# Optimization experiments

Measured on AMD Instinct MI355X. Metric: run time of the kernel, lower is better.

## Reference

```python
import jax, jax.numpy as jnp
import numpy as np

DIM = 4096
N_HEADS_Q = 32
N_HEADS_KV = 8
N_REP = N_HEADS_Q // N_HEADS_KV
HEAD_DIM = DIM // N_HEADS_Q


def setup_inputs() -> dict:
    key = jax.random.key(0)
    k0, k1, k2, k3, k4 = jax.random.split(key, 5)
    B, S = 2, 2048
    scale = 1.0 / np.sqrt(DIM)
    return {
        "x": jax.random.normal(k0, (B, S, DIM), dtype=jnp.float32),
        "wq": jax.random.normal(k1, (DIM, N_HEADS_Q * HEAD_DIM), dtype=jnp.float32) * scale,
        "wk": jax.random.normal(k2, (DIM, N_HEADS_KV * HEAD_DIM), dtype=jnp.float32) * scale,
        "wv": jax.random.normal(k3, (DIM, N_HEADS_KV * HEAD_DIM), dtype=jnp.float32) * scale,
        "wo": jax.random.normal(k4, (DIM, DIM), dtype=jnp.float32) * scale,
        "start_pos": 0,
    }


def reference(x, wq, wk, wv, wo, start_pos):
    # use_cache=False path: fresh causal self-attention with GQA.
    B, S, _ = x.shape
    q = (x @ wq).reshape(B, S, N_HEADS_Q, HEAD_DIM)
    k = (x @ wk).reshape(B, S, N_HEADS_KV, HEAD_DIM)
    v = (x @ wv).reshape(B, S, N_HEADS_KV, HEAD_DIM)
    # repeat_kv: each kv head repeated N_REP times contiguously along head axis
    k = jnp.repeat(k, N_REP, axis=2)  # [B, S, Hq, D]
    v = jnp.repeat(v, N_REP, axis=2)
    att = jnp.einsum("bqhd,bkhd->bhqk", q, k) / np.sqrt(HEAD_DIM).astype(np.float32)
    causal = jnp.tril(jnp.ones((S, S), dtype=bool))  # [S, S]
    att = jnp.where(causal[None, None, :, :], att, -jnp.inf)
    scores = jax.nn.softmax(att, axis=-1)
    out = jnp.einsum("bhqk,bkhd->bqhd", scores, v).reshape(B, S, DIM)
    return out @ wo
```

## Files before the change

kernel.cpp:

```cpp
#include <hip/hip_runtime.h>
#include <cstdint>


typedef __bf16 bf16;
typedef __bf16 bf16x8 __attribute__((ext_vector_type(8)));
typedef float f32x4 __attribute__((ext_vector_type(4)));

#define DEV_INLINE __device__ __forceinline__

DEV_INLINE void load_lds16(const bf16* g, bf16* l) {
  __builtin_amdgcn_global_load_lds(
      (const __attribute__((address_space(1))) void*)g,
      (__attribute__((address_space(3))) void*)l, 16, 0, 0);
}

__global__ __launch_bounds__(256) void cast_f32_bf16(const float* __restrict__ in,
                                                     bf16* __restrict__ out, int n) {
  int i = (blockIdx.x * 256 + threadIdx.x) * 8;
  if (i >= n) return;
  float4 a = *(const float4*)(in + i);
  float4 b = *(const float4*)(in + i + 4);
  bf16x8 o;
  o[0] = (bf16)a.x; o[1] = (bf16)a.y; o[2] = (bf16)a.z; o[3] = (bf16)a.w;
  o[4] = (bf16)b.x; o[5] = (bf16)b.y; o[6] = (bf16)b.z; o[7] = (bf16)b.w;
  *(bf16x8*)(out + i) = o;
}

__global__ __launch_bounds__(256) void transpose_cast_all(
    const float* __restrict__ wq, const float* __restrict__ wk,
    const float* __restrict__ wv, const float* __restrict__ wo,
    bf16* __restrict__ wt, bf16* __restrict__ wot, float qscale) {
  __shared__ float t[32][33];
  int bx = blockIdx.x, k0 = blockIdx.y * 32;
  const float* src;
  bf16* dst;
  int N, ncol0, nrow0;
  float scale = 1.0f;
  if (bx < 128) {
    src = wq; dst = wt; N = 4096; ncol0 = bx * 32; nrow0 = ncol0; scale = qscale;
  } else if (bx < 160) {
    src = wk; dst = wt; N = 1024; ncol0 = (bx - 128) * 32; nrow0 = 4096 + ncol0;
  } else if (bx < 192) {
    src = wv; dst = wt; N = 1024; ncol0 = (bx - 160) * 32; nrow0 = 5120 + ncol0;
  } else {
    src = wo; dst = wot; N = 4096; ncol0 = (bx - 192) * 32; nrow0 = ncol0;
  }
  int tx = threadIdx.x, ty = threadIdx.y;
#pragma unroll
  for (int i = 0; i < 32; i += 8)
    t[ty + i][tx] = src[(size_t)(k0 + ty + i) * N + ncol0 + tx];
  __syncthreads();
#pragma unroll
  for (int i = 0; i < 32; i += 8)
    dst[(size_t)(nrow0 + ty + i) * 4096 + k0 + tx] = (bf16)(t[tx][ty + i] * scale);
}

__global__ __launch_bounds__(256) void transpose_v(const bf16* __restrict__ qkv,
                                                   bf16* __restrict__ vt) {
  __shared__ bf16 t[32][33];
  int s0 = blockIdx.x * 32, d0 = blockIdx.y * 32, bh = blockIdx.z;
  int b = bh >> 3, h = bh & 7;
  int tx = threadIdx.x, ty = threadIdx.y;
#pragma unroll
  for (int i = 0; i < 32; i += 8)
    t[ty + i][tx] =
        qkv[(size_t)(b * 2048 + s0 + ty + i) * 6144 + 5120 + h * 128 + d0 + tx];
  __syncthreads();
#pragma unroll
  for (int i = 0; i < 32; i += 8)
    vt[((size_t)bh * 128 + d0 + ty + i) * 2048 + s0 + tx] = t[tx][ty + i];
}

template <typename OT>
__global__ __launch_bounds__(512, 2) void gemm_bt8(const bf16* __restrict__ A,
                                                   const bf16* __restrict__ Bt,
                                                   OT* __restrict__ C,
                                                   int M, int N, int K) {
  __shared__ __align__(16) bf16 lds[2][4][128 * 64];
  const int t = threadIdx.x, w = t >> 6, l = t & 63;
  const int lr = l & 15, lh = l >> 4;
  const int rm = w >> 2, cn = w & 3;
  const int mBase = blockIdx.y * 256, nBase = blockIdx.x * 256;
  const int NT = K >> 6;

  size_t gA0[2], gB0[2];
#pragma unroll
  for (int it = 0; it < 2; it++) {
    int c = it * 512 + t;
    int idx = c >> 3;
    int kc = (c & 7) ^ (idx & 7);
    gA0[it] = (size_t)(mBase + (idx >> 6) * 128 + (idx & 63)) * K + kc * 8;
    gB0[it] = (size_t)(nBase + (idx >> 5) * 64 + (idx & 31)) * K + kc * 8;
  }
  const size_t strideA1 = (size_t)64 * K;
  const size_t strideB1 = (size_t)32 * K;
  const int ldst0 = (w * 64) * 8, ldst1 = (512 + w * 64) * 8;

#define STAGE_Q(tile, q, base, off0, off1)                                  \
  do {                                                                      \
    int th_ = (tile);                                                       \
    if (th_ < NT) {                                                         \
      bf16* qb_ = &lds[th_ & 1][q][0];                                      \
      size_t ka_ = (size_t)th_ * 64;                                        \
      load_lds16((base) + (off0) + ka_, qb_ + ldst0);                       \
      load_lds16((base) + (off1) + ka_, qb_ + ldst1);                       \
    }                                                                       \
  } while (0)
#define STAGE_A0(tile) STAGE_Q(tile, 0, A, gA0[0], gA0[1])
#define STAGE_B0(tile) STAGE_Q(tile, 1, Bt, gB0[0], gB0[1])
#define STAGE_B1(tile) STAGE_Q(tile, 2, Bt, gB0[0] + strideB1, gB0[1] + strideB1)
#define STAGE_A1(tile) STAGE_Q(tile, 3, A, gA0[0] + strideA1, gA0[1] + strideA1)

  STAGE_A0(0); STAGE_B0(0); STAGE_B1(0); STAGE_A1(0);
  STAGE_A0(1); STAGE_B0(1); STAGE_B1(1);

  f32x4 acc[8][4] = {};
  bf16x8 aF[4][2], bF[4][2];
  const int rowA = (rm * 64 + lr) * 64;
  const int colB = (cn * 32 + lr) * 64;
  const int xo0 = ((lh ^ (lr & 7)) << 3);
  const int xo1 = (((4 + lh) ^ (lr & 7)) << 3);

  for (int T = 0; T < NT; T++) {
    if (T < NT - 1) asm volatile("s_waitcnt vmcnt(6)" ::: "memory");
    else            asm volatile("s_waitcnt vmcnt(0)" ::: "memory");
    __builtin_amdgcn_s_barrier();
    const bf16* q0 = &lds[T & 1][0][0];
    const bf16* q1 = &lds[T & 1][1][0];
    const bf16* q2 = &lds[T & 1][2][0];
    const bf16* q3 = &lds[T & 1][3][0];

#pragma unroll
    for (int mi = 0; mi < 4; mi++) {
      aF[mi][0] = *(const bf16x8*)(q0 + rowA + mi * 1024 + xo0);
      aF[mi][1] = *(const bf16x8*)(q0 + rowA + mi * 1024 + xo1);
    }
#pragma unroll
    for (int ni = 0; ni < 2; ni++) {
      bF[ni][0] = *(const bf16x8*)(q1 + colB + ni * 1024 + xo0);
      bF[ni][1] = *(const bf16x8*)(q1 + colB + ni * 1024 + xo1);
    }
    STAGE_A1(T + 1);
    asm volatile("s_waitcnt lgkmcnt(8)" ::: "memory");
    __builtin_amdgcn_s_barrier();
    asm volatile("s_waitcnt lgkmcnt(0)" ::: "memory");
    __builtin_amdgcn_sched_barrier(0);
    __builtin_amdgcn_s_setprio(1);
#pragma unroll
    for (int mi = 0; mi < 4; mi++)
#pragma unroll
      for (int ni = 0; ni < 2; ni++) {
        acc[mi][ni] = __builtin_amdgcn_mfma_f32_16x16x32_bf16(aF[mi][0], bF[ni][0], acc[mi][ni], 0, 0, 0);
        acc[mi][ni] = __builtin_amdgcn_mfma_f32_16x16x32_bf16(aF[mi][1], bF[ni][1], acc[mi][ni], 0, 0, 0);
      }
    __builtin_amdgcn_s_setprio(0);
    __builtin_amdgcn_s_barrier();

#pragma unroll
    for (int ni = 0; ni < 2; ni++) {
      bF[2 + ni][0] = *(const bf16x8*)(q2 + colB + ni * 1024 + xo0);
      bF[2 + ni][1] = *(const bf16x8*)(q2 + colB + ni * 1024 + xo1);
    }
    STAGE_A0(T + 2);
    __builtin_amdgcn_s_barrier();
    asm volatile("s_waitcnt lgkmcnt(0)" ::: "memory");
    __builtin_amdgcn_sched_barrier(0);
    __builtin_amdgcn_s_setprio(1);
#pragma unroll
    for (int mi = 0; mi < 4; mi++)
#pragma unroll
      for (int ni = 2; ni < 4; ni++) {
        acc[mi][ni] = __builtin_amdgcn_mfma_f32_16x16x32_bf16(aF[mi][0], bF[ni][0], acc[mi][ni], 0, 0, 0);
        acc[mi][ni] = __builtin_amdgcn_mfma_f32_16x16x32_bf16(aF[mi][1], bF[ni][1], acc[mi][ni], 0, 0, 0);
      }
    __builtin_amdgcn_s_setprio(0);
    __builtin_amdgcn_s_barrier();

#pragma unroll
    for (int mi = 0; mi < 4; mi++) {
      aF[mi][0] = *(const bf16x8*)(q3 + rowA + mi * 1024 + xo0);
      aF[mi][1] = *(const bf16x8*)(q3 + rowA + mi * 1024 + xo1);
    }
    STAGE_B0(T + 2);
    __builtin_amdgcn_s_barrier();
    asm volatile("s_waitcnt lgkmcnt(0)" ::: "memory");
    __builtin_amdgcn_sched_barrier(0);
    __builtin_amdgcn_s_setprio(1);
#pragma unroll
    for (int mi = 0; mi < 4; mi++)
#pragma unroll
      for (int ni = 0; ni < 2; ni++) {
        acc[4 + mi][ni] = __builtin_amdgcn_mfma_f32_16x16x32_bf16(aF[mi][0], bF[ni][0], acc[4 + mi][ni], 0, 0, 0);
        acc[4 + mi][ni] = __builtin_amdgcn_mfma_f32_16x16x32_bf16(aF[mi][1], bF[ni][1], acc[4 + mi][ni], 0, 0, 0);
      }
    __builtin_amdgcn_s_setprio(0);
    __builtin_amdgcn_s_barrier();

    STAGE_B1(T + 2);
    __builtin_amdgcn_s_barrier();
    __builtin_amdgcn_s_setprio(1);
#pragma unroll
    for (int mi = 0; mi < 4; mi++)
#pragma unroll
      for (int ni = 2; ni < 4; ni++) {
        acc[4 + mi][ni] = __builtin_amdgcn_mfma_f32_16x16x32_bf16(aF[mi][0], bF[ni][0], acc[4 + mi][ni], 0, 0, 0);
        acc[4 + mi][ni] = __builtin_amdgcn_mfma_f32_16x16x32_bf16(aF[mi][1], bF[ni][1], acc[4 + mi][ni], 0, 0, 0);
      }
    __builtin_amdgcn_s_setprio(0);
    __builtin_amdgcn_s_barrier();
  }
#undef STAGE_Q
#undef STAGE_A0
#undef STAGE_B0
#undef STAGE_B1
#undef STAGE_A1

#pragma unroll
  for (int mi = 0; mi < 8; mi++)
#pragma unroll
    for (int ni = 0; ni < 4; ni++) {
      int row = mBase + rm * 128 + mi * 16 + lh * 4;
      int col = nBase + cn * 64 + ni * 16 + lr;
#pragma unroll
      for (int r = 0; r < 4; r++)
        C[(size_t)(row + r) * N + col] = (OT)acc[mi][ni][r];
    }
}

__global__ __launch_bounds__(256, 2) void flash_attn(const bf16* __restrict__ qkv,
                                                     const bf16* __restrict__ vt,
                                                     bf16* __restrict__ ao) {
  __shared__ __align__(16) bf16 Ks[2][64 * 128];
  __shared__ __align__(16) bf16 Vts[2][128 * 64];
  __shared__ __align__(16) bf16 Ps[4][32 * 64];
  const int t = threadIdx.x, w = t >> 6, l = t & 63;
  const int lr = l & 15, lh = l >> 4;
  const int h = blockIdx.y, b = blockIdx.z;
  const int hkv = h >> 2;

#define STAGE_KV(kt_, buf_)                                                   \
  do {                                                                        \
    const int kb_ = (kt_) * 64;                                               \
    _Pragma("unroll")                                                         \
    for (int p = 0; p < 4; p++) {                                             \
      int c = p * 256 + t;                                                    \
      int ldsoff = (p * 256 + w * 64) * 8;                                    \
      int krow = c >> 4, kj = (c & 15) ^ (krow & 15);                         \
      load_lds16(qkv + (size_t)(b * 2048 + kb_ + krow) * 6144 + 4096 +        \
                     hkv * 128 + kj * 8,                                      \
                 &Ks[buf_][ldsoff]);                                          \
      int vrow = c >> 3, vj = (c & 7) ^ (vrow & 7);                           \
      load_lds16(vt + ((size_t)(b * 8 + hkv) * 128 + vrow) * 2048 + kb_ +     \
                     vj * 8,                                                  \
                 &Vts[buf_][ldsoff]);                                         \
    }                                                                         \
  } while (0)

  for (int phase = 0; phase < 2; phase++) {
    const int qt = phase == 0 ? blockIdx.x : 15 - blockIdx.x;
    const int qrow0 = qt * 128 + w * 32;
    const int nkt = 2 * qt + 2;

    STAGE_KV(0, 0);

    bf16x8 qf[2][4];
#pragma unroll
    for (int rt = 0; rt < 2; rt++)
#pragma unroll
      for (int ds = 0; ds < 4; ds++)
        qf[rt][ds] = *(const bf16x8*)&qkv[(size_t)(b * 2048 + qrow0 + rt * 16 + lr) * 6144 +
                                          h * 128 + ds * 32 + lh * 8];

    f32x4 oacc[2][8] = {};
    float mrow[2][4], lsum[2][4];
#pragma unroll
    for (int rt = 0; rt < 2; rt++)
#pragma unroll
      for (int r = 0; r < 4; r++) { mrow[rt][r] = -3.0e38f; lsum[rt][r] = 0.f; }

    asm volatile("s_waitcnt vmcnt(0)" ::: "memory");
    __builtin_amdgcn_s_barrier();

    for (int kt = 0; kt < nkt; kt++) {
      const int cur = kt & 1;
      const int kbase = kt * 64;
      if (kt + 1 < nkt) STAGE_KV(kt + 1, cur ^ 1);

      f32x4 s[2][4];
      __builtin_amdgcn_s_setprio(1);
#pragma unroll
      for (int ct = 0; ct < 4; ct++) {
        bf16x8 kf[4];
#pragma unroll
        for (int ds = 0; ds < 4; ds++)
          kf[ds] = *(const bf16x8*)&Ks[cur][((ct * 16 + lr) * 16 + ((ds * 4 + lh) ^ lr)) * 8];
#pragma unroll
        for (int rt = 0; rt < 2; rt++) {
          f32x4 acc = {0.f, 0.f, 0.f, 0.f};
#pragma unroll
          for (int ds = 0; ds < 4; ds++)
            acc = __builtin_amdgcn_mfma_f32_16x16x32_bf16(qf[rt][ds], kf[ds], acc, 0, 0, 0);
          s[rt][ct] = acc;
        }
      }
      __builtin_amdgcn_s_setprio(0);

      if (kt >= 2 * qt) {
#pragma unroll
        for (int rt = 0; rt < 2; rt++)
#pragma unroll
          for (int ct = 0; ct < 4; ct++)
#pragma unroll
            for (int r = 0; r < 4; r++) {
              int qi = qrow0 + rt * 16 + lh * 4 + r;
              int ki = kbase + ct * 16 + lr;
              if (ki > qi) s[rt][ct][r] = -3.0e38f;
            }
      }

      float alpha[2][4];
#pragma unroll
      for (int rt = 0; rt < 2; rt++)
#pragma unroll
        for (int r = 0; r < 4; r++) {
          float mx = fmaxf(fmaxf(s[rt][0][r], s[rt][1][r]),
                           fmaxf(s[rt][2][r], s[rt][3][r]));
          mx = fmaxf(mx, __shfl_xor(mx, 1));
          mx = fmaxf(mx, __shfl_xor(mx, 2));
          mx = fmaxf(mx, __shfl_xor(mx, 4));
          mx = fmaxf(mx, __shfl_xor(mx, 8));
          float mnew = fmaxf(mrow[rt][r], mx);
          float al = exp2f(mrow[rt][r] - mnew);
          mrow[rt][r] = mnew;
          alpha[rt][r] = al;
          float rs = 0.f;
#pragma unroll
          for (int ct = 0; ct < 4; ct++) {
            float p = exp2f(s[rt][ct][r] - mnew);
            s[rt][ct][r] = p;
            rs += p;
          }
          rs += __shfl_xor(rs, 1);
          rs += __shfl_xor(rs, 2);
          rs += __shfl_xor(rs, 4);
          rs += __shfl_xor(rs, 8);
          lsum[rt][r] = lsum[rt][r] * al + rs;
        }

#pragma unroll
      for (int rt = 0; rt < 2; rt++)
#pragma unroll
        for (int dt = 0; dt < 8; dt++)
#pragma unroll
          for (int r = 0; r < 4; r++) oacc[rt][dt][r] *= alpha[rt][r];

#pragma unroll
      for (int rt = 0; rt < 2; rt++)
#pragma unroll
        for (int ct = 0; ct < 4; ct++)
#pragma unroll
          for (int r = 0; r < 4; r++) {
            int row = rt * 16 + lh * 4 + r;
            int col = ct * 16 + lr;
            Ps[w][row * 64 + ((((col >> 3) ^ (row & 7)) << 3) | (col & 7))] =
                (bf16)s[rt][ct][r];
          }
      bf16x8 pf[2][2];
#pragma unroll
      for (int rt = 0; rt < 2; rt++)
#pragma unroll
        for (int ks = 0; ks < 2; ks++)
          pf[rt][ks] = *(const bf16x8*)&Ps[w][(rt * 16 + lr) * 64 +
                                              (((ks * 4 + lh) ^ (lr & 7)) << 3)];

      __builtin_amdgcn_s_setprio(1);
#pragma unroll
      for (int dt = 0; dt < 8; dt++)
#pragma unroll
        for (int ks = 0; ks < 2; ks++) {
          bf16x8 vf = *(const bf16x8*)&Vts[cur][((dt * 16 + lr) * 8 +
                                                 ((ks * 4 + lh) ^ (lr & 7))) * 8];
#pragma unroll
          for (int rt = 0; rt < 2; rt++)
            oacc[rt][dt] =
                __builtin_amdgcn_mfma_f32_16x16x32_bf16(pf[rt][ks], vf, oacc[rt][dt], 0, 0, 0);
        }
      __builtin_amdgcn_s_setprio(0);

      asm volatile("s_waitcnt vmcnt(0)" ::: "memory");
      __builtin_amdgcn_s_barrier();
    }

#pragma unroll
    for (int rt = 0; rt < 2; rt++)
#pragma unroll
      for (int dt = 0; dt < 8; dt++)
#pragma unroll
        for (int r = 0; r < 4; r++) {
          float o = oacc[rt][dt][r] / lsum[rt][r];
          int row = b * 2048 + qrow0 + rt * 16 + lh * 4 + r;
          int col = h * 128 + dt * 16 + lr;
          ao[(size_t)row * 4096 + col] = (bf16)o;
        }
  }
#undef STAGE_KV
}

extern "C" void kernel_launch(void* const* d_in, const int* in_sizes, int n_in,
                              void* d_out, int out_size, void* d_ws, size_t ws_size,
                              hipStream_t stream) {
  const float* x = (const float*)d_in[0];
  const float* wq = (const float*)d_in[1];
  const float* wk = (const float*)d_in[2];
  const float* wv = (const float*)d_in[3];
  const float* wo = (const float*)d_in[4];
  float* out = (float*)d_out;

  char* ws = (char*)d_ws;
  bf16* xb = (bf16*)(ws + 0);
  bf16* wt = (bf16*)(ws + 33554432);
  bf16* wot = (bf16*)(ws + 83886080);
  bf16* qkv = (bf16*)(ws + 117440512);
  bf16* vt = (bf16*)(ws + 167772160);
  bf16* ao = (bf16*)(ws + 176160768);
  if (ws_size < 209715200u) return;

  const float qscale = 0.08838834764831845f * 1.4426950408889634f;

  cast_f32_bf16<<<8192, 256, 0, stream>>>(x, xb, 16777216);
  transpose_cast_all<<<dim3(320, 128), dim3(32, 8), 0, stream>>>(
      wq, wk, wv, wo, wt, wot, qscale);

  gemm_bt8<bf16><<<dim3(24, 16), 512, 0, stream>>>(xb, wt, qkv, 4096, 6144, 4096);
  transpose_v<<<dim3(64, 4, 16), dim3(32, 8), 0, stream>>>(qkv, vt);
  flash_attn<<<dim3(8, 32, 2), 256, 0, stream>>>(qkv, vt, ao);
  gemm_bt8<float><<<dim3(16, 16), 512, 0, stream>>>(ao, wot, out, 4096, 4096, 4096);
}
```

Baseline: 790.3 us.

## Rewrite flash attention with transposed 32x32x16 MFMA and register-resident P

Restructures the attention inner loop to compute S^T = K·Q^T with 32x32x16 bf16 MFMAs, so each lane owns one query row. Row max and sum become mostly in-register reductions plus a single cross-half shuffle. P is repacked into MFMA operand layout with lane shuffles, which removes the per-warp LDS round trip. Output stores become 4-wide vectors. The cost is larger accumulators (f32x16 per tile), which adds register pressure at two blocks per CU.

Result: faster. 686.6 us (-13.1%).

```diff
diff --git a/kernel.cpp b/kernel.cpp
--- a/kernel.cpp
+++ b/kernel.cpp
@@ -3,8 +3,10 @@
 
 
 typedef __bf16 bf16;
+typedef __bf16 bf16x4 __attribute__((ext_vector_type(4)));
 typedef __bf16 bf16x8 __attribute__((ext_vector_type(8)));
 typedef float f32x4 __attribute__((ext_vector_type(4)));
+typedef float f32x16 __attribute__((ext_vector_type(16)));
 
 #define DEV_INLINE __device__ __forceinline__
 
@@ -12,6 +14,12 @@
   __builtin_amdgcn_global_load_lds(
       (const __attribute__((address_space(1))) void*)g,
       (__attribute__((address_space(3))) void*)l, 16, 0, 0);
+}
+
+DEV_INLINE unsigned pk2(float a, float b) {
+  union { bf16 v[2]; unsigned u; } t;
+  t.v[0] = (bf16)a; t.v[1] = (bf16)b;
+  return t.u;
 }
 
 __global__ __launch_bounds__(256) void cast_f32_bf16(const float* __restrict__ in,
@@ -232,9 +240,8 @@
                                                      bf16* __restrict__ ao) {
   __shared__ __align__(16) bf16 Ks[2][64 * 128];
   __shared__ __align__(16) bf16 Vts[2][128 * 64];
-  __shared__ __align__(16) bf16 Ps[4][32 * 64];
   const int t = threadIdx.x, w = t >> 6, l = t & 63;
-  const int lr = l & 15, lh = l >> 4;
+  const int l31 = l & 31, hi = l >> 5;
   const int h = blockIdx.y, b = blockIdx.z;
   const int hkv = h >> 2;
 
@@ -260,23 +267,18 @@
     const int qt = phase == 0 ? blockIdx.x : 15 - blockIdx.x;
     const int qrow0 = qt * 128 + w * 32;
     const int nkt = 2 * qt + 2;
+    const int q = qrow0 + l31;
 
     STAGE_KV(0, 0);
 
-    bf16x8 qf[2][4];
-#pragma unroll
-    for (int rt = 0; rt < 2; rt++)
-#pragma unroll
-      for (int ds = 0; ds < 4; ds++)
-        qf[rt][ds] = *(const bf16x8*)&qkv[(size_t)(b * 2048 + qrow0 + rt * 16 + lr) * 6144 +
-                                          h * 128 + ds * 32 + lh * 8];
-
-    f32x4 oacc[2][8] = {};
-    float mrow[2][4], lsum[2][4];
-#pragma unroll
-    for (int rt = 0; rt < 2; rt++)
-#pragma unroll
-      for (int r = 0; r < 4; r++) { mrow[rt][r] = -3.0e38f; lsum[rt][r] = 0.f; }
+    bf16x8 qf[8];
+#pragma unroll
+    for (int d0 = 0; d0 < 8; d0++)
+      qf[d0] = *(const bf16x8*)&qkv[(size_t)(b * 2048 + q) * 6144 + h * 128 +
+                                    d0 * 16 + hi * 8];
+
+    f32x16 oacc[4] = {};
+    float mrow = -3.0e38f, lsum = 0.f;
 
     asm volatile("s_waitcnt vmcnt(0)" ::: "memory");
     __builtin_amdgcn_s_barrier();
@@ -286,122 +288,106 @@
       const int kbase = kt * 64;
       if (kt + 1 < nkt) STAGE_KV(kt + 1, cur ^ 1);
 
-      f32x4 s[2][4];
+      f32x16 s[2] = {};
       __builtin_amdgcn_s_setprio(1);
 #pragma unroll
-      for (int ct = 0; ct < 4; ct++) {
-        bf16x8 kf[4];
-#pragma unroll
-        for (int ds = 0; ds < 4; ds++)
-          kf[ds] = *(const bf16x8*)&Ks[cur][((ct * 16 + lr) * 16 + ((ds * 4 + lh) ^ lr)) * 8];
-#pragma unroll
-        for (int rt = 0; rt < 2; rt++) {
-          f32x4 acc = {0.f, 0.f, 0.f, 0.f};
-#pragma unroll
-          for (int ds = 0; ds < 4; ds++)
-            acc = __builtin_amdgcn_mfma_f32_16x16x32_bf16(qf[rt][ds], kf[ds], acc, 0, 0, 0);
-          s[rt][ct] = acc;
-        }
-      }
-      __builtin_amdgcn_s_setprio(0);
-
-      if (kt >= 2 * qt) {
-#pragma unroll
-        for (int rt = 0; rt < 2; rt++)
-#pragma unroll
-          for (int ct = 0; ct < 4; ct++)
-#pragma unroll
-            for (int r = 0; r < 4; r++) {
-              int qi = qrow0 + rt * 16 + lh * 4 + r;
-              int ki = kbase + ct * 16 + lr;
-              if (ki > qi) s[rt][ct][r] = -3.0e38f;
-            }
-      }
-
-      float alpha[2][4];
-#pragma unroll
-      for (int rt = 0; rt < 2; rt++)
-#pragma unroll
-        for (int r = 0; r < 4; r++) {
-          float mx = fmaxf(fmaxf(s[rt][0][r], s[rt][1][r]),
-                           fmaxf(s[rt][2][r], s[rt][3][r]));
-          mx = fmaxf(mx, __shfl_xor(mx, 1));
-          mx = fmaxf(mx, __shfl_xor(mx, 2));
-          mx = fmaxf(mx, __shfl_xor(mx, 4));
-          mx = fmaxf(mx, __shfl_xor(mx, 8));
-          float mnew = fmaxf(mrow[rt][r], mx);
-          float al = exp2f(mrow[rt][r] - mnew);
-          mrow[rt][r] = mnew;
-          alpha[rt][r] = al;
-          float rs = 0.f;
-#pragma unroll
-          for (int ct = 0; ct < 4; ct++) {
-            float p = exp2f(s[rt][ct][r] - mnew);
-            s[rt][ct][r] = p;
-            rs += p;
-          }
-          rs += __shfl_xor(rs, 1);
-          rs += __shfl_xor(rs, 2);
-          rs += __shfl_xor(rs, 4);
-          rs += __shfl_xor(rs, 8);
-          lsum[rt][r] = lsum[rt][r] * al + rs;
-        }
-
-#pragma unroll
-      for (int rt = 0; rt < 2; rt++)
-#pragma unroll
-        for (int dt = 0; dt < 8; dt++)
-#pragma unroll
-          for (int r = 0; r < 4; r++) oacc[rt][dt][r] *= alpha[rt][r];
-
-#pragma unroll
-      for (int rt = 0; rt < 2; rt++)
-#pragma unroll
-        for (int ct = 0; ct < 4; ct++)
-#pragma unroll
-          for (int r = 0; r < 4; r++) {
-            int row = rt * 16 + lh * 4 + r;
-            int col = ct * 16 + lr;
-            Ps[w][row * 64 + ((((col >> 3) ^ (row & 7)) << 3) | (col & 7))] =
-                (bf16)s[rt][ct][r];
-          }
-      bf16x8 pf[2][2];
-#pragma unroll
-      for (int rt = 0; rt < 2; rt++)
-#pragma unroll
-        for (int ks = 0; ks < 2; ks++)
-          pf[rt][ks] = *(const bf16x8*)&Ps[w][(rt * 16 + lr) * 64 +
-                                              (((ks * 4 + lh) ^ (lr & 7)) << 3)];
-
-      __builtin_amdgcn_s_setprio(1);
-#pragma unroll
-      for (int dt = 0; dt < 8; dt++)
-#pragma unroll
-        for (int ks = 0; ks < 2; ks++) {
-          bf16x8 vf = *(const bf16x8*)&Vts[cur][((dt * 16 + lr) * 8 +
-                                                 ((ks * 4 + lh) ^ (lr & 7))) * 8];
-#pragma unroll
-          for (int rt = 0; rt < 2; rt++)
-            oacc[rt][dt] =
-                __builtin_amdgcn_mfma_f32_16x16x32_bf16(pf[rt][ks], vf, oacc[rt][dt], 0, 0, 0);
+      for (int d0 = 0; d0 < 8; d0++)
+#pragma unroll
+        for (int ct = 0; ct < 2; ct++) {
+          int krow = ct * 32 + l31;
+          bf16x8 kf = *(const bf16x8*)&Ks[cur][(krow * 16 +
+                                                ((d0 * 2 + hi) ^ (krow & 15))) * 8];
+          s[ct] = __builtin_amdgcn_mfma_f32_32x32x16_bf16(kf, qf[d0], s[ct], 0, 0, 0);
         }
       __builtin_amdgcn_s_setprio(0);
 
+      if (kt >= 2 * qt) {
+#pragma unroll
+        for (int ct = 0; ct < 2; ct++)
+#pragma unroll
+          for (int reg = 0; reg < 16; reg++) {
+            int ki = kbase + ct * 32 + (reg & 3) + 8 * (reg >> 2) + 4 * hi;
+            if (ki > q) s[ct][reg] = -3.0e38f;
+          }
+      }
+
+      float tm[16];
+#pragma unroll
+      for (int i = 0; i < 16; i++) tm[i] = fmaxf(s[0][i], s[1][i]);
+#pragma unroll
+      for (int st = 8; st > 0; st >>= 1)
+#pragma unroll
+        for (int i = 0; i < 8; i++)
+          if (i < st) tm[i] = fmaxf(tm[i], tm[i + st]);
+      float mx = fmaxf(tm[0], __shfl_xor(tm[0], 32));
+      float mnew = fmaxf(mrow, mx);
+      float al = exp2f(mrow - mnew);
+      mrow = mnew;
+#pragma unroll
+      for (int ct = 0; ct < 2; ct++)
+#pragma unroll
+        for (int reg = 0; reg < 16; reg++) s[ct][reg] = exp2f(s[ct][reg] - mnew);
+      float ts[16];
+#pragma unroll
+      for (int i = 0; i < 16; i++) ts[i] = s[0][i] + s[1][i];
+#pragma unroll
+      for (int st = 8; st > 0; st >>= 1)
+#pragma unroll
+        for (int i = 0; i < 8; i++)
+          if (i < st) ts[i] = ts[i] + ts[i + st];
+      float rs = ts[0] + __shfl_xor(ts[0], 32);
+      lsum = lsum * al + rs;
+
+#pragma unroll
+      for (int db = 0; db < 4; db++)
+#pragma unroll
+        for (int reg = 0; reg < 16; reg++) oacc[db][reg] *= al;
+
+      bf16x8 pb[4];
+#pragma unroll
+      for (int ks = 0; ks < 4; ks++) {
+        const int ct = ks >> 1, s1 = ks & 1;
+        unsigned A0 = pk2(s[ct][(2 * s1) * 4 + 0], s[ct][(2 * s1) * 4 + 1]);
+        unsigned A1 = pk2(s[ct][(2 * s1) * 4 + 2], s[ct][(2 * s1) * 4 + 3]);
+        unsigned B0 = pk2(s[ct][(2 * s1 + 1) * 4 + 0], s[ct][(2 * s1 + 1) * 4 + 1]);
+        unsigned B1 = pk2(s[ct][(2 * s1 + 1) * 4 + 2], s[ct][(2 * s1 + 1) * 4 + 3]);
+        unsigned z0 = hi ? A0 : B0, z1 = hi ? A1 : B1;
+        unsigned x0 = __shfl_xor(z0, 32), x1 = __shfl_xor(z1, 32);
+        union { unsigned u[4]; bf16x8 v; } pw;
+        pw.u[0] = hi ? x0 : A0;
+        pw.u[1] = hi ? x1 : A1;
+        pw.u[2] = hi ? B0 : x0;
+        pw.u[3] = hi ? B1 : x1;
+        pb[ks] = pw.v;
+      }
+
+      __builtin_amdgcn_s_setprio(1);
+#pragma unroll
+      for (int ks = 0; ks < 4; ks++)
+#pragma unroll
+        for (int db = 0; db < 4; db++) {
+          int vr = db * 32 + l31;
+          bf16x8 vf = *(const bf16x8*)&Vts[cur][(vr * 8 +
+                                                 ((ks * 2 + hi) ^ (vr & 7))) * 8];
+          oacc[db] = __builtin_amdgcn_mfma_f32_32x32x16_bf16(vf, pb[ks], oacc[db], 0, 0, 0);
+        }
+      __builtin_amdgcn_s_setprio(0);
+
       asm volatile("s_waitcnt vmcnt(0)" ::: "memory");
       __builtin_amdgcn_s_barrier();
     }
 
-#pragma unroll
-    for (int rt = 0; rt < 2; rt++)
-#pragma unroll
-      for (int dt = 0; dt < 8; dt++)
-#pragma unroll
-        for (int r = 0; r < 4; r++) {
-          float o = oacc[rt][dt][r] / lsum[rt][r];
-          int row = b * 2048 + qrow0 + rt * 16 + lh * 4 + r;
-          int col = h * 128 + dt * 16 + lr;
-          ao[(size_t)row * 4096 + col] = (bf16)o;
-        }
+    float inv = 1.0f / lsum;
+#pragma unroll
+    for (int db = 0; db < 4; db++)
+#pragma unroll
+      for (int q4 = 0; q4 < 4; q4++) {
+        bf16x4 o4;
+#pragma unroll
+        for (int j = 0; j < 4; j++) o4[j] = (bf16)(oacc[db][q4 * 4 + j] * inv);
+        int d0 = db * 32 + q4 * 8 + hi * 4;
+        *(bf16x4*)&ao[(size_t)(b * 2048 + q) * 4096 + h * 128 + d0] = o4;
+      }
   }
 #undef STAGE_KV
 }
```
